# Kernel optimization log

Hardware: AMD Instinct MI355X
Metric: run time of the kernel (lower is better)

## Reference

```python
import jax, jax.numpy as jnp
import numpy as np


def _pairwise_sq_dists(p, t):
    # p: [N,3], t: [M,3] -> [N,M] squared euclidean distances
    # |p|^2 + |t|^2 - 2 p.t^T (avoids materializing [N,M,3])
    p2 = jnp.sum(p * p, axis=-1)  # [N]
    t2 = jnp.sum(t * t, axis=-1)  # [M]
    cross = jnp.einsum('nd,md->nm', p, t)  # [N,M]
    d = p2[:, None] + t2[None, :] - 2.0 * cross
    return jnp.maximum(d, 0.0)  # clamp tiny negatives from cancellation


def setup_inputs() -> dict:
    key = jax.random.key(0)
    k1, k2 = jax.random.split(key)
    N = 16384
    predict = jax.random.normal(k1, (1, N, 3), dtype=jnp.float32)
    target = jax.random.normal(k2, (1, N, 3), dtype=jnp.float32)
    return {"predict": predict, "target": target}


def reference(predict, target):
    # Faithful to forward: only the first batch element is used.
    p = predict[0]  # [N,3]
    t = target[0]   # [M,3]
    d = _pairwise_sq_dists(p, t)          # [N,M] squared distances
    dist1 = jnp.min(d, axis=1)            # nearest target for each predict pt
    dist2 = jnp.min(d, axis=0)            # nearest predict for each target pt
    loss = jnp.mean(dist1) + jnp.mean(dist2)
    return loss
```

## Files before the change

kernel.cpp:

```cpp
#include <hip/hip_runtime.h>


typedef short s16x8 __attribute__((ext_vector_type(8)));
typedef float f32x16 __attribute__((ext_vector_type(16)));

static __device__ __forceinline__ unsigned short f2bf(float f) {
    unsigned u = __float_as_uint(f);
    unsigned r = (u + 0x7FFFu + ((u >> 16) & 1u)) >> 16;
    return (unsigned short)r;
}
static __device__ __forceinline__ float bf2f(unsigned short h) {
    return __uint_as_float(((unsigned)h) << 16);
}
static __device__ __forceinline__ void split2(float v, unsigned short& h, unsigned short& l) {
    h = f2bf(v);
    l = f2bf(v - bf2f(h));
}
static __device__ __forceinline__ float colmin16(f32x16 v) {
    float a = fminf(v[0], v[1]),  b = fminf(v[2], v[3]);
    float c = fminf(v[4], v[5]),  d = fminf(v[6], v[7]);
    float e = fminf(v[8], v[9]),  f = fminf(v[10], v[11]);
    float g = fminf(v[12], v[13]), h = fminf(v[14], v[15]);
    return fminf(fminf(fminf(a, b), fminf(c, d)),
                 fminf(fminf(e, f), fminf(g, h)));
}

union Pack16 { unsigned short u[16]; uint4 v[2]; };

#define CG  16
#define NRB 64
#define RB  32

__global__ void prep_pack(const float* __restrict__ predict, const float* __restrict__ target,
                          unsigned short* __restrict__ ApP, unsigned short* __restrict__ BpT,
                          unsigned* __restrict__ ticket, int N)
{
    int i = blockIdx.x * blockDim.x + threadIdx.x;
    if (i == 0) *ticket = 0u;
    if (i >= 2 * N) return;
    const unsigned short one = f2bf(1.0f);

    if (i < N) {
        float x = predict[3*i], y = predict[3*i+1], z = predict[3*i+2];
        float n2 = __builtin_fmaf(x, x, __builtin_fmaf(y, y, z*z));
        unsigned short xh,xl,yh,yl,zh,zl,nh,nl;
        split2(x, xh, xl); split2(y, yh, yl); split2(z, zh, zl); split2(n2, nh, nl);
        Pack16 a;
        a.u[0]=xh; a.u[1]=xh; a.u[2]=xl; a.u[3]=xl;
        a.u[4]=yh; a.u[5]=yh; a.u[6]=yl; a.u[7]=yl;
        a.u[8]=zh; a.u[9]=zh; a.u[10]=zl; a.u[11]=zl;
        a.u[12]=nh; a.u[13]=nl; a.u[14]=one; a.u[15]=one;
        uint4* ad = (uint4*)(ApP + (size_t)i * 16);
        ad[0] = a.v[0]; ad[1] = a.v[1];
    } else {
        int j = i - N;
        float x = target[3*j], y = target[3*j+1], z = target[3*j+2];
        float n2 = __builtin_fmaf(x, x, __builtin_fmaf(y, y, z*z));
        unsigned short nh,nl,qxh,qxl,qyh,qyl,qzh,qzl;
        split2(n2, nh, nl);
        split2(-2.0f*x, qxh, qxl); split2(-2.0f*y, qyh, qyl); split2(-2.0f*z, qzh, qzl);
        Pack16 b;
        b.u[0]=qxh; b.u[1]=qxl; b.u[2]=qxh; b.u[3]=qxl;
        b.u[4]=qyh; b.u[5]=qyl; b.u[6]=qyh; b.u[7]=qyl;
        b.u[8]=qzh; b.u[9]=qzl; b.u[10]=qzh; b.u[11]=qzl;
        b.u[12]=one; b.u[13]=one; b.u[14]=nh; b.u[15]=nl;
        uint4* bd = (uint4*)(BpT + (size_t)j * 16);
        bd[0] = b.v[0]; bd[1] = b.v[1];
    }
}

__global__ __launch_bounds__(256, 4) void chamfer_main(
    const unsigned short* __restrict__ Ap, const unsigned short* __restrict__ Bp,
    float* __restrict__ partials1, float* __restrict__ cpart, int N)
{
    __shared__ float cm[4][1024];

    const int tid  = threadIdx.x;
    const int w    = tid >> 6;
    const int lane = tid & 63;
    const int lm   = lane & 31;
    const int lg   = lane >> 5;
    const int bx   = blockIdx.x;
    const int cg   = blockIdx.y;

    const int row0 = bx * 256 + w * 64;

    const uint4* A4 = (const uint4*)Ap;
    s16x8 a0 = __builtin_bit_cast(s16x8, A4[(size_t)(row0      + lm) * 2 + lg]);
    s16x8 a1 = __builtin_bit_cast(s16x8, A4[(size_t)(row0 + 32 + lm) * 2 + lg]);

    float rm0[16], rm1[16];
    #pragma unroll
    for (int r = 0; r < 16; ++r) { rm0[r] = 3.0e38f; rm1[r] = 3.0e38f; }

    const f32x16 zc = {0.f,0.f,0.f,0.f,0.f,0.f,0.f,0.f,0.f,0.f,0.f,0.f,0.f,0.f,0.f,0.f};

    const int npt = N / CG;
    const int NT  = npt / 32;
    const uint4* bp = (const uint4*)Bp + (size_t)cg * npt * 2 + lm * 2 + lg;
    float* cmw = cm[w];

    uint4 c0 = bp[0];
    uint4 c1 = bp[64];
    const uint4* bnext = bp + 128;

#define BODY(TT)                                                              \
    {                                                                         \
        s16x8 bA = __builtin_bit_cast(s16x8, c0);                             \
        s16x8 bB = __builtin_bit_cast(s16x8, c1);                             \
        f32x16 p0 = __builtin_amdgcn_mfma_f32_32x32x16_bf16(a0, bA, zc, 0,0,0);\
        f32x16 q0 = __builtin_amdgcn_mfma_f32_32x32x16_bf16(a0, bB, zc, 0,0,0);\
        f32x16 p1 = __builtin_amdgcn_mfma_f32_32x32x16_bf16(a1, bA, zc, 0,0,0);\
        f32x16 q1 = __builtin_amdgcn_mfma_f32_32x32x16_bf16(a1, bB, zc, 0,0,0);\
        _Pragma("unroll")                                                     \
        for (int r = 0; r < 16; ++r) {                                        \
            rm0[r] = fminf(fminf(rm0[r], p0[r]), q0[r]);                      \
            rm1[r] = fminf(fminf(rm1[r], p1[r]), q1[r]);                      \
        }                                                                     \
        float va = fminf(colmin16(p0), colmin16(p1));                         \
        va = fminf(va, __shfl_xor(va, 32, 64));                               \
        float vb = fminf(colmin16(q0), colmin16(q1));                         \
        vb = fminf(vb, __shfl_xor(vb, 32, 64));                               \
        if (lane < 32) {                                                      \
            cmw[(TT) * 32 + lm]      = va;                                    \
            cmw[(TT) * 32 + 32 + lm] = vb;                                    \
        }                                                                     \
    }

    int t = 0;
    for (; t < NT - 2; t += 2) {
        uint4 n0 = bnext[0];
        uint4 n1 = bnext[64];
        bnext += 128;
        BODY(t);
        c0 = n0; c1 = n1;
    }
    BODY(t);
#undef BODY

    #pragma unroll
    for (int m = 1; m <= 16; m <<= 1) {
        #pragma unroll
        for (int r = 0; r < 16; ++r) {
            rm0[r] = fminf(rm0[r], __shfl_xor(rm0[r], m, 64));
            rm1[r] = fminf(rm1[r], __shfl_xor(rm1[r], m, 64));
        }
    }
    float* __restrict__ pout = partials1 + (size_t)cg * N;
    #pragma unroll
    for (int r = 0; r < 16; ++r) {
        int rl = (r & 3) + 8 * (r >> 2) + 4 * lg;
        if (lm == r) {
            pout[row0 +      rl] = rm0[r];
            pout[row0 + 32 + rl] = rm1[r];
        }
    }

    __syncthreads();
    float* __restrict__ crow = cpart + (size_t)bx * N + (size_t)cg * npt;
    for (int c = tid; c < npt; c += 256) {
        float m = fminf(fminf(cm[0][c], cm[1][c]), fminf(cm[2][c], cm[3][c]));
        crow[c] = m;
    }
}

__global__ void chamfer_reduce(const float* __restrict__ partials1,
                               const float* __restrict__ cpart,
                               double* __restrict__ bsum, unsigned* __restrict__ ticket,
                               float* __restrict__ out, int N)
{
    const int n4 = N >> 2;
    const float4* p4 = (const float4*)partials1;
    const float4* c4 = (const float4*)cpart;
    double acc = 0.0;
    for (int i = blockIdx.x * blockDim.x + threadIdx.x; i < n4;
         i += gridDim.x * blockDim.x) {
        float4 m = p4[i];
        #pragma unroll
        for (int g = 1; g < CG; ++g) {
            float4 v = p4[(size_t)g * n4 + i];
            m.x = fminf(m.x, v.x); m.y = fminf(m.y, v.y);
            m.z = fminf(m.z, v.z); m.w = fminf(m.w, v.w);
        }
        acc += (double)fmaxf(m.x, 0.0f) + (double)fmaxf(m.y, 0.0f)
             + (double)fmaxf(m.z, 0.0f) + (double)fmaxf(m.w, 0.0f);

        float4 mc = c4[i];
        for (int g = 1; g < NRB; ++g) {
            float4 v = c4[(size_t)g * n4 + i];
            mc.x = fminf(mc.x, v.x); mc.y = fminf(mc.y, v.y);
            mc.z = fminf(mc.z, v.z); mc.w = fminf(mc.w, v.w);
        }
        acc += (double)fmaxf(mc.x, 0.0f) + (double)fmaxf(mc.y, 0.0f)
             + (double)fmaxf(mc.z, 0.0f) + (double)fmaxf(mc.w, 0.0f);
    }
    for (int off = 32; off; off >>= 1)
        acc += __shfl_down(acc, off, 64);
    __shared__ double sacc[4];
    const int wave = threadIdx.x >> 6, lane = threadIdx.x & 63;
    if (lane == 0) sacc[wave] = acc;
    __syncthreads();

    __shared__ unsigned is_last;
    if (threadIdx.x == 0) {
        bsum[blockIdx.x] = sacc[0] + sacc[1] + sacc[2] + sacc[3];
        __threadfence();
        unsigned old = atomicAdd(ticket, 1u);
        is_last = (old == gridDim.x - 1u) ? 1u : 0u;
    }
    __syncthreads();
    if (!is_last) return;

    if (threadIdx.x == 0) {
        __threadfence();
        double t = 0.0;
        for (int i = 0; i < RB; ++i) t += bsum[i];
        out[0] = (float)(t / (double)N);
    }
}

extern "C" void kernel_launch(void* const* d_in, const int* in_sizes, int n_in,
                              void* d_out, int out_size, void* d_ws, size_t ws_size,
                              hipStream_t stream) {
    const float* predict = (const float*)d_in[0];
    const float* target  = (const float*)d_in[1];
    const int N = in_sizes[0] / 3;

    unsigned short* ws16 = (unsigned short*)d_ws;
    unsigned short* ApP = ws16;
    unsigned short* BpT = ws16 + (size_t)1 * N * 16;
    float* partials1 = (float*)(ws16 + (size_t)2 * N * 16);
    float* cpart = partials1 + (size_t)CG * N;
    double* bsum = (double*)(cpart + (size_t)NRB * N);
    unsigned* ticket = (unsigned*)(bsum + RB);

    prep_pack<<<dim3((2 * N + 255) / 256), dim3(256), 0, stream>>>(
        predict, target, ApP, BpT, ticket, N);

    dim3 grid(N / 256, CG);
    chamfer_main<<<grid, dim3(256), 0, stream>>>(ApP, BpT, partials1, cpart, N);

    chamfer_reduce<<<dim3(RB), dim3(256), 0, stream>>>(
        partials1, cpart, bsum, ticket, (float*)d_out, N);
}
```

Baseline: 93.03 us.

## Replace partial-min buffers and reduce kernel with atomicMin and last-block sum

Row and column minima now go straight into a single 2N array of float bit patterns using atomicMin on non-negative values. A ticket lets the last finishing block sum that array, which removes the separate reduce kernel and the large partial buffers. The in-wave column reduction no longer uses a cross-half shuffle: each half-wave writes its own shared-memory slice, so LDS doubles and occupancy bounds drop from 4 to 2 blocks. The cost is global atomic contention, and the final sum now runs serially in one block.

```diff
diff --git a/kernel.cpp b/kernel.cpp
--- a/kernel.cpp
+++ b/kernel.cpp
@@ -16,28 +16,31 @@
     h = f2bf(v);
     l = f2bf(v - bf2f(h));
 }
-static __device__ __forceinline__ float colmin16(f32x16 v) {
-    float a = fminf(v[0], v[1]),  b = fminf(v[2], v[3]);
-    float c = fminf(v[4], v[5]),  d = fminf(v[6], v[7]);
-    float e = fminf(v[8], v[9]),  f = fminf(v[10], v[11]);
-    float g = fminf(v[12], v[13]), h = fminf(v[14], v[15]);
-    return fminf(fminf(fminf(a, b), fminf(c, d)),
-                 fminf(fminf(e, f), fminf(g, h)));
+static __device__ __forceinline__ float colmin32(f32x16 p, f32x16 q) {
+    float v[32];
+    #pragma unroll
+    for (int r = 0; r < 16; ++r) { v[r] = p[r]; v[16 + r] = q[r]; }
+    #pragma unroll
+    for (int s = 16; s >= 1; s >>= 1) {
+        #pragma unroll
+        for (int i = 0; i < s; ++i) v[i] = fminf(v[i], v[i + s]);
+    }
+    return v[0];
 }
 
 union Pack16 { unsigned short u[16]; uint4 v[2]; };
 
-#define CG  16
-#define NRB 64
-#define RB  32
+#define CG 16
 
 __global__ void prep_pack(const float* __restrict__ predict, const float* __restrict__ target,
                           unsigned short* __restrict__ ApP, unsigned short* __restrict__ BpT,
-                          unsigned* __restrict__ ticket, int N)
+                          unsigned* __restrict__ minbits, unsigned* __restrict__ ticket,
+                          int N)
 {
     int i = blockIdx.x * blockDim.x + threadIdx.x;
     if (i == 0) *ticket = 0u;
     if (i >= 2 * N) return;
+    minbits[i] = 0x7F7FFFFFu;
     const unsigned short one = f2bf(1.0f);
 
     if (i < N) {
@@ -69,11 +72,12 @@
     }
 }
 
-__global__ __launch_bounds__(256, 4) void chamfer_main(
+__global__ __launch_bounds__(256, 2) void chamfer_main(
     const unsigned short* __restrict__ Ap, const unsigned short* __restrict__ Bp,
-    float* __restrict__ partials1, float* __restrict__ cpart, int N)
+    unsigned* __restrict__ minbits, unsigned* __restrict__ ticket,
+    float* __restrict__ out, int N)
 {
-    __shared__ float cm[4][1024];
+    __shared__ float cm[4][2048];
 
     const int tid  = threadIdx.x;
     const int w    = tid >> 6;
@@ -98,7 +102,7 @@
     const int npt = N / CG;
     const int NT  = npt / 32;
     const uint4* bp = (const uint4*)Bp + (size_t)cg * npt * 2 + lm * 2 + lg;
-    float* cmw = cm[w];
+    float* cmw = cm[w] + lg * 1024;
 
     uint4 c0 = bp[0];
     uint4 c1 = bp[64];
@@ -117,14 +121,8 @@
             rm0[r] = fminf(fminf(rm0[r], p0[r]), q0[r]);                      \
             rm1[r] = fminf(fminf(rm1[r], p1[r]), q1[r]);                      \
         }                                                                     \
-        float va = fminf(colmin16(p0), colmin16(p1));                         \
-        va = fminf(va, __shfl_xor(va, 32, 64));                               \
-        float vb = fminf(colmin16(q0), colmin16(q1));                         \
-        vb = fminf(vb, __shfl_xor(vb, 32, 64));                               \
-        if (lane < 32) {                                                      \
-            cmw[(TT) * 32 + lm]      = va;                                    \
-            cmw[(TT) * 32 + 32 + lm] = vb;                                    \
-        }                                                                     \
+        cmw[(TT) * 32 + lm]     = colmin32(p0, p1);                           \
+        cmw[(TT + 1) * 32 + lm] = colmin32(q0, q1);                           \
     }
 
     int t = 0;
@@ -146,77 +144,52 @@
             rm1[r] = fminf(rm1[r], __shfl_xor(rm1[r], m, 64));
         }
     }
-    float* __restrict__ pout = partials1 + (size_t)cg * N;
     #pragma unroll
     for (int r = 0; r < 16; ++r) {
         int rl = (r & 3) + 8 * (r >> 2) + 4 * lg;
         if (lm == r) {
-            pout[row0 +      rl] = rm0[r];
-            pout[row0 + 32 + rl] = rm1[r];
+            atomicMin(&minbits[row0 +      rl], __float_as_uint(fmaxf(rm0[r], 0.0f)));
+            atomicMin(&minbits[row0 + 32 + rl], __float_as_uint(fmaxf(rm1[r], 0.0f)));
         }
     }
 
     __syncthreads();
-    float* __restrict__ crow = cpart + (size_t)bx * N + (size_t)cg * npt;
+    unsigned* __restrict__ cbits = minbits + N + (size_t)cg * npt;
     for (int c = tid; c < npt; c += 256) {
-        float m = fminf(fminf(cm[0][c], cm[1][c]), fminf(cm[2][c], cm[3][c]));
-        crow[c] = m;
-    }
-}
-
-__global__ void chamfer_reduce(const float* __restrict__ partials1,
-                               const float* __restrict__ cpart,
-                               double* __restrict__ bsum, unsigned* __restrict__ ticket,
-                               float* __restrict__ out, int N)
-{
-    const int n4 = N >> 2;
-    const float4* p4 = (const float4*)partials1;
-    const float4* c4 = (const float4*)cpart;
+        float m = fminf(fminf(fminf(cm[0][c], cm[0][1024 + c]),
+                              fminf(cm[1][c], cm[1][1024 + c])),
+                        fminf(fminf(cm[2][c], cm[2][1024 + c]),
+                              fminf(cm[3][c], cm[3][1024 + c])));
+        atomicMin(&cbits[c], __float_as_uint(fmaxf(m, 0.0f)));
+    }
+
+    __threadfence();
+    __shared__ unsigned is_last;
+    if (tid == 0) {
+        unsigned total = gridDim.x * gridDim.y;
+        unsigned old = atomicAdd(ticket, 1u);
+        is_last = (old == total - 1u) ? 1u : 0u;
+    }
+    __syncthreads();
+    if (!is_last) return;
+    __threadfence();
+
+    const uint4* mb4 = (const uint4*)minbits;
+    const int n4 = (2 * N) >> 2;
     double acc = 0.0;
-    for (int i = blockIdx.x * blockDim.x + threadIdx.x; i < n4;
-         i += gridDim.x * blockDim.x) {
-        float4 m = p4[i];
-        #pragma unroll
-        for (int g = 1; g < CG; ++g) {
-            float4 v = p4[(size_t)g * n4 + i];
-            m.x = fminf(m.x, v.x); m.y = fminf(m.y, v.y);
-            m.z = fminf(m.z, v.z); m.w = fminf(m.w, v.w);
-        }
-        acc += (double)fmaxf(m.x, 0.0f) + (double)fmaxf(m.y, 0.0f)
-             + (double)fmaxf(m.z, 0.0f) + (double)fmaxf(m.w, 0.0f);
-
-        float4 mc = c4[i];
-        for (int g = 1; g < NRB; ++g) {
-            float4 v = c4[(size_t)g * n4 + i];
-            mc.x = fminf(mc.x, v.x); mc.y = fminf(mc.y, v.y);
-            mc.z = fminf(mc.z, v.z); mc.w = fminf(mc.w, v.w);
-        }
-        acc += (double)fmaxf(mc.x, 0.0f) + (double)fmaxf(mc.y, 0.0f)
-             + (double)fmaxf(mc.z, 0.0f) + (double)fmaxf(mc.w, 0.0f);
+    #pragma unroll 4
+    for (int i = tid; i < n4; i += 256) {
+        uint4 v = mb4[i];
+        acc += (double)__uint_as_float(v.x) + (double)__uint_as_float(v.y)
+             + (double)__uint_as_float(v.z) + (double)__uint_as_float(v.w);
     }
     for (int off = 32; off; off >>= 1)
         acc += __shfl_down(acc, off, 64);
     __shared__ double sacc[4];
-    const int wave = threadIdx.x >> 6, lane = threadIdx.x & 63;
-    if (lane == 0) sacc[wave] = acc;
+    if (lane == 0) sacc[w] = acc;
     __syncthreads();
-
-    __shared__ unsigned is_last;
-    if (threadIdx.x == 0) {
-        bsum[blockIdx.x] = sacc[0] + sacc[1] + sacc[2] + sacc[3];
-        __threadfence();
-        unsigned old = atomicAdd(ticket, 1u);
-        is_last = (old == gridDim.x - 1u) ? 1u : 0u;
-    }
-    __syncthreads();
-    if (!is_last) return;
-
-    if (threadIdx.x == 0) {
-        __threadfence();
-        double t = 0.0;
-        for (int i = 0; i < RB; ++i) t += bsum[i];
-        out[0] = (float)(t / (double)N);
-    }
+    if (tid == 0)
+        out[0] = (float)((sacc[0] + sacc[1] + sacc[2] + sacc[3]) / (double)N);
 }
 
 extern "C" void kernel_launch(void* const* d_in, const int* in_sizes, int n_in,
@@ -229,17 +202,13 @@
     unsigned short* ws16 = (unsigned short*)d_ws;
     unsigned short* ApP = ws16;
     unsigned short* BpT = ws16 + (size_t)1 * N * 16;
-    float* partials1 = (float*)(ws16 + (size_t)2 * N * 16);
-    float* cpart = partials1 + (size_t)CG * N;
-    double* bsum = (double*)(cpart + (size_t)NRB * N);
-    unsigned* ticket = (unsigned*)(bsum + RB);
+    unsigned* minbits = (unsigned*)(ws16 + (size_t)2 * N * 16);
+    unsigned* ticket  = minbits + (size_t)2 * N;
 
     prep_pack<<<dim3((2 * N + 255) / 256), dim3(256), 0, stream>>>(
-        predict, target, ApP, BpT, ticket, N);
+        predict, target, ApP, BpT, minbits, ticket, N);
 
     dim3 grid(N / 256, CG);
-    chamfer_main<<<grid, dim3(256), 0, stream>>>(ApP, BpT, partials1, cpart, N);
-
-    chamfer_reduce<<<dim3(RB), dim3(256), 0, stream>>>(
-        partials1, cpart, bsum, ticket, (float*)d_out, N);
-}
+    chamfer_main<<<grid, dim3(256), 0, stream>>>(
+        ApP, BpT, minbits, ticket, (float*)d_out, N);
+}
```

After: 138.0 us. 48.3% more time.
